# Kernel tuning notes

Measured on AMD Instinct MI355X. Metric: run time of the kernel, lower is better.

Reference implementation:

```python
import jax, jax.numpy as jnp
import numpy as np


def setup_inputs() -> dict:
    key = jax.random.key(0)
    k1, k2, k3 = jax.random.split(key, 3)
    inp = jax.random.normal(k1, (32, 128, 56, 56), dtype=jnp.float32)
    # kaiming-style scale for a 3x3 conv kernel
    fan_in = 128 * 3 * 3
    kernel = jax.random.normal(k2, (256, 128, 3, 3), dtype=jnp.float32) * np.float32(np.sqrt(2.0 / fan_in))
    bias = jax.random.normal(k3, (256,), dtype=jnp.float32)
    return {"inp": inp, "kernel": kernel, "bias": bias}


def reference(inp, kernel, bias):
    # 3x3 conv, stride 1, padding 1 (SAME), NCHW / OIHW layout, plus bias.
    out = jax.lax.conv_general_dilated(
        inp, kernel,
        window_strides=(1, 1),
        padding=((1, 1), (1, 1)),
        dimension_numbers=("NCHW", "OIHW", "NCHW"),
    )
    return out + bias[None, :, None, None]
```

## Files before the change

### kernel.cpp

```cpp
#include <hip/hip_runtime.h>
#include <hip/hip_bf16.h>


#define C_IN   128
#define K_OUT  256
#define HW     56
#define IMG    3136
#define NBATCH 32
#define PW     58
#define IN_WS_USHORT ((size_t)4*NBATCH*PW*256*8)
#define WT_WS_USHORT ((size_t)12*2*1536*8)

typedef __bf16 bf16x8 __attribute__((ext_vector_type(8)));
typedef float  f32x4  __attribute__((ext_vector_type(4)));
typedef unsigned short ushort8 __attribute__((ext_vector_type(8)));

__device__ inline unsigned short f2bf(float f) {
    unsigned int u = __builtin_bit_cast(unsigned int, f);
    u += ((u >> 16) & 1u) + 0x7FFFu;
    return (unsigned short)(u >> 16);
}

__device__ __forceinline__ void gl2lds16(const unsigned short* g, unsigned short* l) {
    __builtin_amdgcn_global_load_lds(
        (const __attribute__((address_space(1))) unsigned int*)g,
        (__attribute__((address_space(3))) unsigned int*)l, 16, 0, 0);
}

__global__ void prep_input(const float* __restrict__ inp,
                           unsigned short* __restrict__ dst) {
    __shared__ unsigned short tile[C_IN * 57];
    int n = blockIdx.x / PW, py = blockIdx.x % PW;
    ushort8* d8 = (ushort8*)dst;
    const bool border = (py == 0 || py == PW - 1);
    if (!border) {
        const float* src = inp + (size_t)n * C_IN * IMG + (py - 1) * HW;
        for (int i = threadIdx.x; i < C_IN * HW; i += 256) {
            int c = i / HW, x = i - c * HW;
            tile[c * 57 + x] = f2bf(src[c * IMG + x]);
        }
        __syncthreads();
    }
    for (int i = threadIdx.x; i < 1024; i += 256) {
        int cq = i >> 8, rem = i & 255;
        int X = ((rem >> 6) & 3) * 16 + (rem & 15);
        int cc = (rem >> 4) & 3;
        ushort8 v = (ushort8)0;
        if (!border && X >= 1 && X <= HW) {
#pragma unroll
            for (int e = 0; e < 8; ++e)
                v[e] = tile[(cq * 32 + cc * 8 + e) * 57 + (X - 1)];
        }
        d8[((size_t)(cq * NBATCH + n) * PW + py) * 256 + rem] = v;
    }
}

__global__ void prep_weights(const float* __restrict__ w,
                             unsigned short* __restrict__ dst) {
    int chunk = blockIdx.x * 256 + threadIdx.x;
    int p = chunk / 3072, rem = chunk - p * 3072;
    int koh = rem / 1536, rem2 = rem - koh * 1536;
    int s = rem2 / 512, rem3 = rem2 - s * 512;
    int koq = rem3 >> 6, cc = (rem3 >> 4) & 3, kor = rem3 & 15;
    int ko = koh * 128 + koq * 16 + kor;
    int cq = p / 3, r = p - 3 * cq;
    ushort8 v;
#pragma unroll
    for (int e = 0; e < 8; ++e)
        v[e] = f2bf(w[(ko * C_IN + cq * 32 + cc * 8 + e) * 9 + r * 3 + s]);
    ((ushort8*)dst)[chunk] = v;
}

__global__ __launch_bounds__(256, 2) void conv_mfma(
        const unsigned short* __restrict__ In,
        const unsigned short* __restrict__ Wt,
        const float* __restrict__ bias,
        float* __restrict__ out) {
    __shared__ unsigned short smem[24576];

    const int tid = threadIdx.x;
    const int lane = tid & 63, wv = tid >> 6;
    const int l15 = lane & 15, lk = lane >> 4;
    const int koh = blockIdx.y;
    const int by = blockIdx.x;
    const int n = by / 14, rb = (by % 14) * 4;

    const int wkol = (wv & 1) * 64;
    const int wpx  = (wv >> 1) * 112;
    const int wlane = (wv & 1) * 2048 + lk * 128 + l15 * 8;

    int yl[7], xp[3][7];
#pragma unroll
    for (int nf = 0; nf < 7; ++nf) {
        int p = wpx + nf * 16 + l15;
        yl[nf] = p / 56;
        int x = p - yl[nf] * 56;
#pragma unroll
        for (int s = 0; s < 3; ++s) {
            int X = x + s;
            xp[s][nf] = ((X >> 4) << 10) + lk * 256 + ((X & 15) << 4);
        }
    }

    f32x4 acc[4][7];
#pragma unroll
    for (int m = 0; m < 4; ++m)
#pragma unroll
        for (int nf = 0; nf < 7; ++nf) acc[m][nf] = (f32x4)0.0f;

    bf16x8 wbuf[2][4];

#define LOAD_WS(G_) do {                                                    \
    if constexpr ((G_) <= 35) {                                             \
        constexpr int p_ = (G_) / 3, sx_ = (G_) % 3;                        \
        const unsigned short* wp = Wt + ((size_t)(p_ * 2 + koh)) * 12288    \
                                   + sx_ * 4096 + wlane;                    \
        _Pragma("unroll")                                                   \
        for (int m = 0; m < 4; ++m)                                         \
            wbuf[(G_) & 1][m] = *(const bf16x8*)(wp + m * 512);             \
    } } while (0)

#define STAGE_ROW(C_, T_) do {                                              \
    gl2lds16(In + ((size_t)(((C_) * NBATCH + n) * PW + rb + (T_))) * 2048 + tid * 8, \
             &smem[((6 * (C_) + (T_)) % 12) * 2048 + tid * 8]);             \
} while (0)

#define STEP(PH, S_) do {                                                   \
    constexpr int g_ = (PH) * 3 + (S_);                                     \
    LOAD_WS(g_ + 1);                                                        \
    { const char* ib = (const char*)smem;                                   \
      bf16x8 b[7];                                                          \
      _Pragma("unroll")                                                     \
      for (int nf = 0; nf < 7; ++nf)                                        \
          b[nf] = *(const bf16x8*)(ib + roff[nf] + xp[(S_)][nf]);           \
      __builtin_amdgcn_s_setprio(1);                                        \
      _Pragma("unroll")                                                     \
      for (int m = 0; m < 4; ++m)                                           \
          _Pragma("unroll")                                                 \
          for (int nf = 0; nf < 7; ++nf)                                    \
              acc[m][nf] = __builtin_amdgcn_mfma_f32_16x16x32_bf16(         \
                  wbuf[g_ & 1][m], b[nf], acc[m][nf], 0, 0, 0);             \
      __builtin_amdgcn_s_setprio(0);                                        \
    }                                                                       \
} while (0)

    STAGE_ROW(0, 0); STAGE_ROW(0, 1); STAGE_ROW(0, 2); STAGE_ROW(0, 3);
    asm volatile("" ::: "memory");
    LOAD_WS(0);

#define PHASE(PH) do {                                                      \
    constexpr int cqp_ = (PH) / 3, rp_ = (PH) % 3;                          \
    constexpr int nI_ = (rp_ == 2) ? (cqp_ < 3 ? 2 : 0) : (cqp_ < 3 ? 2 : 1); \
    if constexpr (rp_ == 0) {                                               \
        STAGE_ROW(cqp_, 4);                                                 \
        if constexpr (cqp_ < 3) STAGE_ROW(cqp_ + 1, 0);                     \
    } else if constexpr (rp_ == 1) {                                        \
        STAGE_ROW(cqp_, 5);                                                 \
        if constexpr (cqp_ < 3) STAGE_ROW(cqp_ + 1, 1);                     \
    } else {                                                                \
        if constexpr (cqp_ < 3) { STAGE_ROW(cqp_ + 1, 2); STAGE_ROW(cqp_ + 1, 3); } \
    }                                                                       \
    asm volatile("s_waitcnt vmcnt(%0)" :: "i"(4 + nI_) : "memory");         \
    asm volatile("s_barrier" ::: "memory");                                 \
    { int roff[7];                                                          \
      _Pragma("unroll")                                                     \
      for (int nf = 0; nf < 7; ++nf) {                                      \
          int t = 6 * cqp_ + rp_ + yl[nf];                                  \
          roff[nf] = (t >= 12 ? t - 12 : t) << 12;                          \
      }                                                                     \
      STEP(PH, 0); STEP(PH, 1); STEP(PH, 2);                                \
    }                                                                       \
} while (0)

    PHASE(0);  PHASE(1);  PHASE(2);  PHASE(3);
    PHASE(4);  PHASE(5);  PHASE(6);  PHASE(7);
    PHASE(8);  PHASE(9);  PHASE(10); PHASE(11);

#undef PHASE
#undef STEP
#undef STAGE_ROW
#undef LOAD_WS

    const int sp0 = rb * 56 + wpx;
#pragma unroll
    for (int m = 0; m < 4; ++m) {
        int kb = koh * 128 + wkol + m * 16 + lk * 4;
        f32x4 bs = *(const f32x4*)(bias + kb);
#pragma unroll
        for (int nf = 0; nf < 7; ++nf) {
            float* ob = out + ((size_t)(n * K_OUT + kb) * IMG) + sp0 + nf * 16 + l15;
#pragma unroll
            for (int j = 0; j < 4; ++j)
                ob[(size_t)j * IMG] = acc[m][nf][j] + bs[j];
        }
    }
}

__global__ void conv_naive(const float* __restrict__ inp,
                           const float* __restrict__ ker,
                           const float* __restrict__ bias,
                           float* __restrict__ out, int total) {
    int o = blockIdx.x * blockDim.x + threadIdx.x;
    if (o >= total) return;
    int x = o % HW, y = (o / HW) % HW, ko = (o / IMG) % K_OUT, n = o / (IMG * K_OUT);
    float acc = bias[ko];
    for (int c = 0; c < C_IN; ++c)
        for (int r = 0; r < 3; ++r) {
            int iy = y + r - 1; if ((unsigned)iy >= HW) continue;
            for (int s = 0; s < 3; ++s) {
                int ix = x + s - 1; if ((unsigned)ix >= HW) continue;
                acc += inp[((n * C_IN + c) * HW + iy) * HW + ix]
                     * ker[((ko * C_IN + c) * 3 + r) * 3 + s];
            }
        }
    out[o] = acc;
}

extern "C" void kernel_launch(void* const* d_in, const int* in_sizes, int n_in,
                              void* d_out, int out_size, void* d_ws, size_t ws_size,
                              hipStream_t stream) {
    const float* inp  = (const float*)d_in[0];
    const float* ker  = (const float*)d_in[1];
    const float* bias = (const float*)d_in[2];
    float* out = (float*)d_out;

    const size_t need = (IN_WS_USHORT + WT_WS_USHORT) * 2;
    if (ws_size < need) {
        int total = NBATCH * K_OUT * IMG;
        conv_naive<<<(total + 255) / 256, 256, 0, stream>>>(inp, ker, bias, out, total);
        return;
    }

    unsigned short* inb = (unsigned short*)d_ws;
    unsigned short* wtb = inb + IN_WS_USHORT;

    prep_input<<<NBATCH * PW, 256, 0, stream>>>(inp, inb);
    prep_weights<<<144, 256, 0, stream>>>(ker, wtb);

    conv_mfma<<<dim3(448, 2), 256, 0, stream>>>(inb, wtb, bias, out);
}
```

Baseline: 79.10 us.

## Fuse input bf16 conversion into conv kernel, drop prep_input pass

Removes the separate prep_input kernel that converted and repacked the fp32 input to a padded bf16 layout in workspace. The conv kernel now loads fp32 input rows straight from global memory into registers, converts them to bf16 and writes them to LDS after the MFMA step, with padding handled by predicates. This saves a full extra read/write pass of the activations and one launch. In exchange it replaces async global-to-LDS copies with register staging, adds register pressure, and issues strided per-channel fp32 loads, and both blocks (koh=0,1) now convert the same input.

```diff
diff --git a/kernel.cpp b/kernel.cpp
--- a/kernel.cpp
+++ b/kernel.cpp
@@ -8,7 +8,6 @@
 #define IMG    3136
 #define NBATCH 32
 #define PW     58
-#define IN_WS_USHORT ((size_t)4*NBATCH*PW*256*8)
 #define WT_WS_USHORT ((size_t)12*2*1536*8)
 
 typedef __bf16 bf16x8 __attribute__((ext_vector_type(8)));
@@ -19,40 +18,6 @@
     unsigned int u = __builtin_bit_cast(unsigned int, f);
     u += ((u >> 16) & 1u) + 0x7FFFu;
     return (unsigned short)(u >> 16);
-}
-
-__device__ __forceinline__ void gl2lds16(const unsigned short* g, unsigned short* l) {
-    __builtin_amdgcn_global_load_lds(
-        (const __attribute__((address_space(1))) unsigned int*)g,
-        (__attribute__((address_space(3))) unsigned int*)l, 16, 0, 0);
-}
-
-__global__ void prep_input(const float* __restrict__ inp,
-                           unsigned short* __restrict__ dst) {
-    __shared__ unsigned short tile[C_IN * 57];
-    int n = blockIdx.x / PW, py = blockIdx.x % PW;
-    ushort8* d8 = (ushort8*)dst;
-    const bool border = (py == 0 || py == PW - 1);
-    if (!border) {
-        const float* src = inp + (size_t)n * C_IN * IMG + (py - 1) * HW;
-        for (int i = threadIdx.x; i < C_IN * HW; i += 256) {
-            int c = i / HW, x = i - c * HW;
-            tile[c * 57 + x] = f2bf(src[c * IMG + x]);
-        }
-        __syncthreads();
-    }
-    for (int i = threadIdx.x; i < 1024; i += 256) {
-        int cq = i >> 8, rem = i & 255;
-        int X = ((rem >> 6) & 3) * 16 + (rem & 15);
-        int cc = (rem >> 4) & 3;
-        ushort8 v = (ushort8)0;
-        if (!border && X >= 1 && X <= HW) {
-#pragma unroll
-            for (int e = 0; e < 8; ++e)
-                v[e] = tile[(cq * 32 + cc * 8 + e) * 57 + (X - 1)];
-        }
-        d8[((size_t)(cq * NBATCH + n) * PW + py) * 256 + rem] = v;
-    }
 }
 
 __global__ void prep_weights(const float* __restrict__ w,
@@ -72,7 +37,7 @@
 }
 
 __global__ __launch_bounds__(256, 2) void conv_mfma(
-        const unsigned short* __restrict__ In,
+        const float* __restrict__ inp,
         const unsigned short* __restrict__ Wt,
         const float* __restrict__ bias,
         float* __restrict__ out) {
@@ -88,6 +53,12 @@
     const int wkol = (wv & 1) * 64;
     const int wpx  = (wv >> 1) * 112;
     const int wlane = (wv & 1) * 2048 + lk * 128 + l15 * 8;
+
+    const int Xq_ = tid >> 6, cc_ = (tid >> 4) & 3, Xr_ = tid & 15;
+    const int X_ = Xq_ * 16 + Xr_;
+    const bool xok = (X_ >= 1) & (X_ <= 56);
+    const int xi = xok ? X_ - 1 : 0;
+    const float* ibase = inp + ((size_t)(n * C_IN + cc_ * 8)) * IMG + xi;
 
     int yl[7], xp[3][7];
 #pragma unroll
@@ -120,9 +91,19 @@
             wbuf[(G_) & 1][m] = *(const bf16x8*)(wp + m * 512);             \
     } } while (0)
 
-#define STAGE_ROW(C_, T_) do {                                              \
-    gl2lds16(In + ((size_t)(((C_) * NBATCH + n) * PW + rb + (T_))) * 2048 + tid * 8, \
-             &smem[((6 * (C_) + (T_)) % 12) * 2048 + tid * 8]);             \
+#define ILOAD(C_, T_, D_) do {                                              \
+    int py_ = rb + (T_);                                                    \
+    bool ok_ = xok & (py_ >= 1) & (py_ <= 56);                              \
+    const float* bp_ = ibase + (size_t)(C_) * 32 * IMG + (py_ - 1) * 56;    \
+    _Pragma("unroll")                                                       \
+    for (int e = 0; e < 8; ++e) D_[e] = ok_ ? bp_[e * IMG] : 0.0f;          \
+} while (0)
+
+#define IWRITE(C_, T_, D_) do {                                             \
+    ushort8 v_;                                                             \
+    _Pragma("unroll")                                                       \
+    for (int e = 0; e < 8; ++e) v_[e] = f2bf(D_[e]);                        \
+    *(ushort8*)&smem[(((6 * (C_) + (T_)) % 12) * 2048) + tid * 8] = v_;     \
 } while (0)
 
 #define STEP(PH, S_) do {                                                   \
@@ -144,24 +125,28 @@
     }                                                                       \
 } while (0)
 
-    STAGE_ROW(0, 0); STAGE_ROW(0, 1); STAGE_ROW(0, 2); STAGE_ROW(0, 3);
-    asm volatile("" ::: "memory");
+    {
+        float p0[8], p1[8], p2[8], p3[8];
+        ILOAD(0, 0, p0); ILOAD(0, 1, p1); ILOAD(0, 2, p2); ILOAD(0, 3, p3);
+        IWRITE(0, 0, p0); IWRITE(0, 1, p1); IWRITE(0, 2, p2); IWRITE(0, 3, p3);
+    }
     LOAD_WS(0);
+    asm volatile("s_waitcnt lgkmcnt(0)" ::: "memory");
+    asm volatile("s_barrier" ::: "memory");
 
 #define PHASE(PH) do {                                                      \
     constexpr int cqp_ = (PH) / 3, rp_ = (PH) % 3;                          \
-    constexpr int nI_ = (rp_ == 2) ? (cqp_ < 3 ? 2 : 0) : (cqp_ < 3 ? 2 : 1); \
+    float s0[8], s1[8];                                                     \
     if constexpr (rp_ == 0) {                                               \
-        STAGE_ROW(cqp_, 4);                                                 \
-        if constexpr (cqp_ < 3) STAGE_ROW(cqp_ + 1, 0);                     \
+        ILOAD(cqp_, 4, s0);                                                 \
+        if constexpr (cqp_ < 3) ILOAD(cqp_ + 1, 0, s1);                     \
     } else if constexpr (rp_ == 1) {                                        \
-        STAGE_ROW(cqp_, 5);                                                 \
-        if constexpr (cqp_ < 3) STAGE_ROW(cqp_ + 1, 1);                     \
-    } else {                                                                \
-        if constexpr (cqp_ < 3) { STAGE_ROW(cqp_ + 1, 2); STAGE_ROW(cqp_ + 1, 3); } \
-    }                                                                       \
-    asm volatile("s_waitcnt vmcnt(%0)" :: "i"(4 + nI_) : "memory");         \
-    asm volatile("s_barrier" ::: "memory");                                 \
+        ILOAD(cqp_, 5, s0);                                                 \
+        if constexpr (cqp_ < 3) ILOAD(cqp_ + 1, 1, s1);                     \
+    } else if constexpr (cqp_ < 3) {                                        \
+        ILOAD(cqp_ + 1, 2, s0); ILOAD(cqp_ + 1, 3, s1);                     \
+    }                                                                       \
+    asm volatile("" ::: "memory");             \
     { int roff[7];                                                          \
       _Pragma("unroll")                                                     \
       for (int nf = 0; nf < 7; ++nf) {                                      \
@@ -170,6 +155,17 @@
       }                                                                     \
       STEP(PH, 0); STEP(PH, 1); STEP(PH, 2);                                \
     }                                                                       \
+    if constexpr (rp_ == 0) {                                               \
+        IWRITE(cqp_, 4, s0);                                                \
+        if constexpr (cqp_ < 3) IWRITE(cqp_ + 1, 0, s1);                    \
+    } else if constexpr (rp_ == 1) {                                        \
+        IWRITE(cqp_, 5, s0);                                                \
+        if constexpr (cqp_ < 3) IWRITE(cqp_ + 1, 1, s1);                    \
+    } else if constexpr (cqp_ < 3) {                                        \
+        IWRITE(cqp_ + 1, 2, s0); IWRITE(cqp_ + 1, 3, s1);                   \
+    }                                                                       \
+    asm volatile("s_waitcnt lgkmcnt(0)" ::: "memory");                      \
+    asm volatile("s_barrier" ::: "memory");                                 \
 } while (0)
 
     PHASE(0);  PHASE(1);  PHASE(2);  PHASE(3);
@@ -178,7 +174,8 @@
 
 #undef PHASE
 #undef STEP
-#undef STAGE_ROW
+#undef IWRITE
+#undef ILOAD
 #undef LOAD_WS
 
     const int sp0 = rb * 56 + wpx;
@@ -224,18 +221,15 @@
     const float* bias = (const float*)d_in[2];
     float* out = (float*)d_out;
 
-    const size_t need = (IN_WS_USHORT + WT_WS_USHORT) * 2;
+    const size_t need = WT_WS_USHORT * 2;
     if (ws_size < need) {
         int total = NBATCH * K_OUT * IMG;
         conv_naive<<<(total + 255) / 256, 256, 0, stream>>>(inp, ker, bias, out, total);
         return;
     }
 
-    unsigned short* inb = (unsigned short*)d_ws;
-    unsigned short* wtb = inb + IN_WS_USHORT;
-
-    prep_input<<<NBATCH * PW, 256, 0, stream>>>(inp, inb);
+    unsigned short* wtb = (unsigned short*)d_ws;
+
     prep_weights<<<144, 256, 0, stream>>>(ker, wtb);
-
-    conv_mfma<<<dim3(448, 2), 256, 0, stream>>>(inb, wtb, bias, out);
-}
+    conv_mfma<<<dim3(448, 2), 256, 0, stream>>>(inp, wtb, bias, out);
+}
```

Result: slower. 118.6 us (+49.9%).
